# Kernel tuning notes

Measured on AMD Instinct MI355X. Metric: run time of the kernel, lower is better.

The kernel has to match this reference:

```python
import jax, jax.numpy as jnp
import numpy as np

BS, SEQ, DIN, HID, H = 2, 2048, 1024, 1024, 16
D = HID // H  # head_size = 64

def setup_inputs() -> dict:
    key = jax.random.key(0)
    ks = jax.random.split(key, 9)
    s = 0.02
    return {
        "x":    jax.random.normal(ks[0], (BS, SEQ, DIN), jnp.float32),
        "Wq":   jax.random.normal(ks[1], (DIN, HID), jnp.float32) * s,
        "bq":   jax.random.normal(ks[2], (HID,), jnp.float32) * s,
        "Wk":   jax.random.normal(ks[3], (DIN, HID), jnp.float32) * s,
        "bk":   jax.random.normal(ks[4], (HID,), jnp.float32) * s,
        "Wv":   jax.random.normal(ks[5], (DIN, HID), jnp.float32) * s,
        "bv":   jax.random.normal(ks[6], (HID,), jnp.float32) * s,
        "Wmix": jax.random.normal(ks[7], (HID, HID), jnp.float32) * s,
        "bmix": jax.random.normal(ks[8], (HID,), jnp.float32) * s,
    }

def reference(x, Wq, bq, Wk, bk, Wv, bv, Wmix, bmix):
    bs, seq, _ = x.shape
    scale = jnp.asarray(D ** 0.5, x.dtype)
    # projections, split heads: [b, s, H, D] (contiguous channel slices per head,
    # equivalent to the torch transpose/reshape dance)
    q = (x @ Wq + bq).reshape(bs, seq, H, D)
    k = (x @ Wk + bk).reshape(bs, seq, H, D)
    v = (x @ Wv + bv).reshape(bs, seq, H, D)
    scores = jnp.einsum('bqhd,bkhd->bhqk', q, k) / scale  # [b, H, seq, seq]
    causal_mask = jnp.triu(jnp.ones((seq, seq), bool), k=1)
    scores = jnp.where(causal_mask, -jnp.inf, scores)
    probs = jax.nn.softmax(scores, axis=-1)
    att = jnp.einsum('bhqk,bkhd->bqhd', probs, v).reshape(bs, seq, HID)
    return att @ Wmix + bmix
```

## Files before the change

kernel.cpp:

```cpp
#include <hip/hip_runtime.h>
#include <hip/hip_bf16.h>

#define BS 2
#define SEQ 2048
#define DIN 1024
#define HID 1024
#define NH 16
#define HD 64
#define M_ROWS (BS*SEQ)
#define NQKV 3072

typedef __attribute__((ext_vector_type(8))) short short8;
typedef __attribute__((ext_vector_type(4))) short short4v;
typedef __attribute__((ext_vector_type(8))) __bf16 bf16x8;
typedef __attribute__((ext_vector_type(4))) float floatx4;

__device__ __forceinline__ short f2bf(float f) {
  return __builtin_bit_cast(short, (__bf16)f);
}
__device__ __forceinline__ float bf2f(short s) {
  return __uint_as_float(((unsigned)(unsigned short)s) << 16);
}

__device__ __forceinline__ floatx4 mfma16(short8 a, short8 b, floatx4 c) {
  return __builtin_amdgcn_mfma_f32_16x16x32_bf16(
      __builtin_bit_cast(bf16x8, a), __builtin_bit_cast(bf16x8, b), c, 0, 0, 0);
}

__device__ __forceinline__ float exp2fast(float x) {
#if __has_builtin(__builtin_amdgcn_exp2f)
  return __builtin_amdgcn_exp2f(x);
#else
  return exp2f(x);
#endif
}

__device__ __forceinline__ void gload_lds16(const void* g, void* l) {
  __builtin_amdgcn_global_load_lds(
      (const __attribute__((address_space(1))) unsigned int*)g,
      (__attribute__((address_space(3))) unsigned int*)l, 16, 0, 0);
}

__device__ __forceinline__ void lds_w8s(short* base, int row, int colsh, short8 v) {
  *(short8*)((char*)base + row * 128 + ((colsh * 2) ^ ((row & 7) << 4))) = v;
}
__device__ __forceinline__ void lds_w4s(short* base, int row, int colsh, short4v v) {
  *(short4v*)((char*)base + row * 128 + ((colsh * 2) ^ ((row & 7) << 4))) = v;
}
__device__ __forceinline__ short8 lds_r8s(const short* base, int row, int colsh) {
  return *(const short8*)((const char*)base + row * 128 + ((colsh * 2) ^ ((row & 7) << 4)));
}

__global__ __launch_bounds__(256) void convx_kernel(const float* __restrict__ x,
                                                    short* __restrict__ xb) {
  int gid = blockIdx.x * 256 + threadIdx.x;
  const float4* x4 = (const float4*)x;
  float4 v0 = x4[2 * gid], v1 = x4[2 * gid + 1];
  short8 o;
  o[0] = f2bf(v0.x); o[1] = f2bf(v0.y); o[2] = f2bf(v0.z); o[3] = f2bf(v0.w);
  o[4] = f2bf(v1.x); o[5] = f2bf(v1.y); o[6] = f2bf(v1.z); o[7] = f2bf(v1.w);
  *(short8*)&xb[(size_t)gid * 8] = o;
}

__global__ __launch_bounds__(256) void transw_kernel(
    const float* __restrict__ Wq, const float* __restrict__ Wk,
    const float* __restrict__ Wv, const float* __restrict__ Wmix,
    short* __restrict__ Wt, short* __restrict__ Wmixt)
{
  __shared__ float Ws[64][65];
  const float* src; short* dst;
  switch (blockIdx.z) {
    case 0:  src = Wq;   dst = Wt;                 break;
    case 1:  src = Wk;   dst = Wt + (1u << 20);    break;
    case 2:  src = Wv;   dst = Wt + (2u << 20);    break;
    default: src = Wmix; dst = Wmixt;              break;
  }
  const int n0 = blockIdx.x * 64, k0 = blockIdx.y * 64;
  const int c = threadIdx.x & 63, r0 = threadIdx.x >> 6;
  #pragma unroll
  for (int i = 0; i < 16; ++i) {
    int rr = r0 + 4 * i;
    Ws[rr][c] = src[(size_t)(k0 + rr) * DIN + n0 + c];
  }
  __syncthreads();
  #pragma unroll
  for (int i = 0; i < 16; ++i) {
    int cc = r0 + 4 * i;
    dst[(size_t)(n0 + cc) * DIN + k0 + c] = f2bf(Ws[c][cc]);
  }
}

template<int BM, int BN, bool OUT_F32, bool QKV>
__global__ __launch_bounds__(256) void gemm_kernel(
    const short* __restrict__ A, const short* __restrict__ Bt,
    const float* __restrict__ bias, void* __restrict__ Cp,
    short* __restrict__ vt, int Ndim, int Kdim)
{
  constexpr int MT = BM / 32, NT = BN / 32;
  __shared__ short As[BM * 64];
  __shared__ short Bs[BN * 64];
  const int tid = threadIdx.x;
  const int wid = tid >> 6, lane = tid & 63, lg = lane >> 4, lm = lane & 15;
  const int wr = wid >> 1, wc = wid & 1;
  const int m0 = blockIdx.y * BM, n0 = blockIdx.x * BN;

  floatx4 acc[MT][NT];
  #pragma unroll
  for (int i = 0; i < MT; ++i)
    #pragma unroll
    for (int j = 0; j < NT; ++j) acc[i][j] = floatx4{0.f, 0.f, 0.f, 0.f};

  for (int k0 = 0; k0 < Kdim; k0 += 64) {
    __syncthreads();
    #pragma unroll
    for (int j = 0; j < BM / 32; ++j) {
      int flat = tid + 256 * j;
      int row = flat >> 3, ch = (flat & 7) ^ (row & 7);
      gload_lds16(A + (size_t)(m0 + row) * Kdim + k0 + ch * 8,
                  (char*)As + wid * 1024 + j * 4096);
    }
    #pragma unroll
    for (int j = 0; j < BN / 32; ++j) {
      int flat = tid + 256 * j;
      int row = flat >> 3, ch = (flat & 7) ^ (row & 7);
      gload_lds16(Bt + (size_t)(n0 + row) * Kdim + k0 + ch * 8,
                  (char*)Bs + wid * 1024 + j * 4096);
    }
    __syncthreads();

    #pragma unroll
    for (int kk = 0; kk < 2; ++kk) {
      short8 a[MT], b[NT];
      #pragma unroll
      for (int mt = 0; mt < MT; ++mt) {
        int row = wr * (BM / 2) + mt * 16 + lm;
        int ch = (kk * 4 + lg) ^ (row & 7);
        a[mt] = *(const short8*)&As[row * 64 + ch * 8];
      }
      #pragma unroll
      for (int nt = 0; nt < NT; ++nt) {
        int row = wc * (BN / 2) + nt * 16 + lm;
        int ch = (kk * 4 + lg) ^ (row & 7);
        b[nt] = *(const short8*)&Bs[row * 64 + ch * 8];
      }
      #pragma unroll
      for (int mt = 0; mt < MT; ++mt)
        #pragma unroll
        for (int nt = 0; nt < NT; ++nt)
          acc[mt][nt] = mfma16(a[mt], b[nt], acc[mt][nt]);
    }
  }

  #pragma unroll
  for (int mt = 0; mt < MT; ++mt) {
    const int row0 = m0 + wr * (BM / 2) + mt * 16 + 4 * lg;
    #pragma unroll
    for (int nt = 0; nt < NT; ++nt) {
      const int col = n0 + wc * (BN / 2) + nt * 16 + lm;
      const float bv = bias[col];
      if (QKV && n0 >= 2048) {
        int hd = col - 2048;
        int bb = row0 >> 11, s = row0 & 2047;
        short4v pv;
        #pragma unroll
        for (int r = 0; r < 4; ++r) pv[r] = f2bf(acc[mt][nt][r] + bv);
        *(short4v*)&vt[((size_t)(bb * (NH * HD) + hd)) * SEQ + s] = pv;
      } else {
        #pragma unroll
        for (int r = 0; r < 4; ++r) {
          float v = acc[mt][nt][r] + bv;
          if (OUT_F32) ((float*)Cp)[(size_t)(row0 + r) * Ndim + col] = v;
          else         ((short*)Cp)[(size_t)(row0 + r) * Ndim + col] = f2bf(v);
        }
      }
    }
  }
}

#define MFIX 12.0f
__global__ __launch_bounds__(256) void attn_kernel(
    const short* __restrict__ qkv, const short* __restrict__ vt,
    short* __restrict__ att, short* __restrict__ pO, float* __restrict__ pml)
{
  __shared__ short Ks[64 * 64];
  __shared__ short Vs[64 * 64];
  __shared__ short Ps[4 * 16 * 64];
  const int tid = threadIdx.x;
  const int wid = tid >> 6, lane = tid & 63, lg = lane >> 4, lm = lane & 15;

  int id = blockIdx.x, x, c;
  if (id < 4)        { x = id;                       c = 0;        }
  else if (id < 12)  { int t = id - 4;   x = 4  + (t >> 1); c = t & 1; }
  else if (id < 24)  { int t = id - 12;  x = 8  + t / 3;    c = t % 3; }
  else if (id < 40)  { int t = id - 24;  x = 12 + (t >> 2); c = t & 3; }
  else if (id < 60)  { int t = id - 40;  x = 16 + t / 5;    c = t % 5; }
  else if (id < 84)  { int t = id - 60;  x = 20 + t / 6;    c = t % 6; }
  else if (id < 112) { int t = id - 84;  x = 24 + t / 7;    c = t % 7; }
  else               { int t = id - 112; x = 28 + (t >> 3); c = t & 7; }
  const int nch = (x >> 2) + 1;
  const int tb = c * 4;
  const int te = min(tb + 4, x + 1);
  const int q0 = x * 64;
  const int bh = blockIdx.y, b = bh >> 4, h = bh & 15;
  const short* qp = qkv + (size_t)(b * SEQ) * NQKV + h * HD;
  const short* kp = qp + HID;
  const short* vp = vt + (size_t)bh * HD * SEQ;

  const float cl2 = 0.18033688011112042f;
  const int qrow_g = q0 + wid * 16 + lm;
  short8 qf[2];
  {
    const short* qrow = qp + (size_t)qrow_g * NQKV;
    #pragma unroll
    for (int kk = 0; kk < 2; ++kk) {
      short8 raw = *(const short8*)(qrow + kk * 32 + lg * 8);
      #pragma unroll
      for (int j = 0; j < 8; ++j) qf[kk][j] = f2bf(bf2f(raw[j]) * cl2);
    }
  }

  short8 ones;
  #pragma unroll
  for (int j = 0; j < 8; ++j) ones[j] = (short)0x3F80;

  const int rstage = tid >> 3, c8 = (tid & 7) * 8;
  short8 kreg[2], vreg[2];
  #pragma unroll
  for (int i = 0; i < 2; ++i) {
    kreg[i] = *(const short8*)(kp + (size_t)(tb * 64 + rstage + 32 * i) * NQKV + c8);
    vreg[i] = *(const short8*)(vp + (size_t)(rstage + 32 * i) * SEQ + tb * 64 + c8);
  }

  short* psw = Ps + wid * 16 * 64;
  floatx4 o[4];
  floatx4 ol = floatx4{0.f, 0.f, 0.f, 0.f};
  #pragma unroll
  for (int nt = 0; nt < 4; ++nt) o[nt] = floatx4{0.f, 0.f, 0.f, 0.f};

  for (int t = tb; t < te; ++t) {
    __syncthreads();
    #pragma unroll
    for (int i = 0; i < 2; ++i) {
      lds_w8s(Ks, rstage + 32 * i, c8, kreg[i]);
      lds_w8s(Vs, rstage + 32 * i, c8, vreg[i]);
    }
    __syncthreads();
    if (t + 1 < te) {
      const int kv1 = (t + 1) * 64;
      #pragma unroll
      for (int i = 0; i < 2; ++i) {
        kreg[i] = *(const short8*)(kp + (size_t)(kv1 + rstage + 32 * i) * NQKV + c8);
        vreg[i] = *(const short8*)(vp + (size_t)(rstage + 32 * i) * SEQ + kv1 + c8);
      }
    }

    floatx4 s[4];
    #pragma unroll
    for (int nt = 0; nt < 4; ++nt) s[nt] = floatx4{-MFIX, -MFIX, -MFIX, -MFIX};
    __builtin_amdgcn_s_setprio(1);
    #pragma unroll
    for (int kk = 0; kk < 2; ++kk)
      #pragma unroll
      for (int nt = 0; nt < 4; ++nt)
        s[nt] = mfma16(lds_r8s(Ks, nt * 16 + lm, kk * 32 + lg * 8), qf[kk], s[nt]);
    __builtin_amdgcn_s_setprio(0);

    if (t == x) {
      #pragma unroll
      for (int nt = 0; nt < 4; ++nt)
        #pragma unroll
        for (int r = 0; r < 4; ++r) {
          int kv = t * 64 + nt * 16 + 4 * lg + r;
          if (kv > qrow_g) s[nt][r] = -3e38f;
        }
    }

    #pragma unroll
    for (int nt = 0; nt < 4; ++nt) {
      short4v pv;
      #pragma unroll
      for (int r = 0; r < 4; ++r) pv[r] = f2bf(exp2fast(s[nt][r]));
      lds_w4s(psw, lm, nt * 16 + 4 * lg, pv);
    }

    #pragma unroll
    for (int kk = 0; kk < 2; ++kk) {
      short8 pf = lds_r8s(psw, lm, kk * 32 + lg * 8);
      __builtin_amdgcn_s_setprio(1);
      #pragma unroll
      for (int nt = 0; nt < 4; ++nt)
        o[nt] = mfma16(lds_r8s(Vs, nt * 16 + lm, kk * 32 + lg * 8), pf, o[nt]);
      ol = mfma16(ones, pf, ol);
      __builtin_amdgcn_s_setprio(0);
    }
  }

  if (nch == 1) {
    const float linv = 1.0f / ol[0];
    #pragma unroll
    for (int nt = 0; nt < 4; ++nt) {
      short4v ov;
      #pragma unroll
      for (int r = 0; r < 4; ++r) ov[r] = f2bf(o[nt][r] * linv);
      *(short4v*)&att[((size_t)(b * SEQ + qrow_g)) * HID + h * HD + nt * 16 + 4 * lg] = ov;
    }
  } else {
    const int g = x >> 2;
    const int slot = bh * 140 + (2 * g * g + 2 * g - 4 + (x & 3) * (g + 1)) + c;
    short* po = pO + (size_t)slot * 4096;
    const int ql = wid * 16 + lm;
    #pragma unroll
    for (int nt = 0; nt < 4; ++nt) {
      short4v ov;
      #pragma unroll
      for (int r = 0; r < 4; ++r) ov[r] = f2bf(o[nt][r]);
      *(short4v*)&po[ql * 64 + nt * 16 + 4 * lg] = ov;
    }
    if (lane < 16) {
      pml[slot * 128 + 64 + ql] = ol[0];
    }
  }
}

__global__ __launch_bounds__(256) void combine_kernel(
    const short* __restrict__ pO, const float* __restrict__ pml,
    short* __restrict__ att)
{
  const int x = 4 + blockIdx.x;
  const int bh = blockIdx.y, b = bh >> 4, h = bh & 15;
  const int g = x >> 2;
  const int nch = g + 1;
  const int tid = threadIdx.x;
  const int row = tid >> 2, d0 = (tid & 3) * 16;
  const int base_slot = bh * 140 + (2 * g * g + 2 * g - 4 + (x & 3) * (g + 1));

  float L = 0.f;
  for (int cc = 0; cc < nch; ++cc)
    L += pml[(base_slot + cc) * 128 + 64 + row];
  const float inv = 1.0f / L;

  float acc[16];
  #pragma unroll
  for (int j = 0; j < 16; ++j) acc[j] = 0.f;
  for (int cc = 0; cc < nch; ++cc) {
    const short* po = pO + (size_t)(base_slot + cc) * 4096 + row * 64 + d0;
    short8 v0 = *(const short8*)po, v1 = *(const short8*)(po + 8);
    #pragma unroll
    for (int j = 0; j < 8; ++j) {
      acc[j]     += bf2f(v0[j]);
      acc[j + 8] += bf2f(v1[j]);
    }
  }
  short8 o0, o1;
  #pragma unroll
  for (int j = 0; j < 8; ++j) {
    o0[j] = f2bf(acc[j] * inv);
    o1[j] = f2bf(acc[j + 8] * inv);
  }
  short* dst = att + ((size_t)(b * SEQ + x * 64 + row)) * HID + h * HD + d0;
  *(short8*)dst = o0;
  *(short8*)(dst + 8) = o1;
}

extern "C" void kernel_launch(void* const* d_in, const int* in_sizes, int n_in,
                              void* d_out, int out_size, void* d_ws, size_t ws_size,
                              hipStream_t stream) {
  (void)in_sizes; (void)n_in; (void)out_size; (void)ws_size;
  const float* x    = (const float*)d_in[0];
  const float* Wq   = (const float*)d_in[1];
  const float* bq   = (const float*)d_in[2];
  const float* Wk   = (const float*)d_in[3];
  const float* bk   = (const float*)d_in[4];
  const float* Wv   = (const float*)d_in[5];
  const float* bv   = (const float*)d_in[6];
  const float* Wmix = (const float*)d_in[7];
  const float* bmix = (const float*)d_in[8];
  float* out = (float*)d_out;

  char* w = (char*)d_ws;
  short* xb      = (short*)w; w += (size_t)8 << 20;
  short* Wt      = (short*)w; w += (size_t)6 << 20;
  short* Wmixt   = (short*)w; w += (size_t)2 << 20;
  float* biascat = (float*)w; w += (size_t)64 << 10;
  short* qkvb    = (short*)w; w += (size_t)24 << 20;
  short* vtb     = (short*)w; w += (size_t)8 << 20;
  short* ab      = (short*)w; w += (size_t)8 << 20;
  short* pO      = (short*)w; w += (size_t)140 * 32 * 4096 * 2;
  float* pml     = (float*)w;

  hipLaunchKernelGGL(convx_kernel, dim3(2048), dim3(256), 0, stream, x, xb);
  hipLaunchKernelGGL(transw_kernel, dim3(16, 16, 4), dim3(256), 0, stream,
                     Wq, Wk, Wv, Wmix, Wt, Wmixt);
  hipMemcpyAsync(biascat,        bq, 1024 * sizeof(float), hipMemcpyDeviceToDevice, stream);
  hipMemcpyAsync(biascat + 1024, bk, 1024 * sizeof(float), hipMemcpyDeviceToDevice, stream);
  hipMemcpyAsync(biascat + 2048, bv, 1024 * sizeof(float), hipMemcpyDeviceToDevice, stream);

  hipLaunchKernelGGL((gemm_kernel<128, 128, false, true>), dim3(NQKV / 128, M_ROWS / 128),
                     dim3(256), 0, stream, xb, Wt, biascat, (void*)qkvb, vtb, NQKV, DIN);

  hipLaunchKernelGGL(attn_kernel, dim3(144, BS * NH), dim3(256), 0, stream,
                     qkvb, vtb, ab, pO, pml);
  hipLaunchKernelGGL(combine_kernel, dim3(28, BS * NH), dim3(256), 0, stream,
                     pO, pml, ab);

  hipLaunchKernelGGL((gemm_kernel<64, 128, true, false>), dim3(HID / 128, M_ROWS / 64),
                     dim3(256), 0, stream, ab, Wmixt, bmix, (void*)out, (short*)nullptr,
                     HID, DIN);
}
```

Baseline: 115.3 us.

## Process two 64-row query tiles per attention block to reuse K/V tiles

Each attention block now handles 128 query rows, split into two 64-row sub-tiles that share every staged K/V tile in LDS. This halves the global K/V loads and LDS staging per query row, and halves the number of partial-output slots and combine blocks. The block index is now decoded by a loop instead of the hard-coded table. In exchange, each block holds twice the accumulators (more register pressure), and there are half as many blocks, so occupancy and load balance across CUs may suffer.

```diff
diff --git a/kernel.cpp b/kernel.cpp
--- a/kernel.cpp
+++ b/kernel.cpp
@@ -188,34 +188,30 @@
   const int tid = threadIdx.x;
   const int wid = tid >> 6, lane = tid & 63, lg = lane >> 4, lm = lane & 15;
 
-  int id = blockIdx.x, x, c;
-  if (id < 4)        { x = id;                       c = 0;        }
-  else if (id < 12)  { int t = id - 4;   x = 4  + (t >> 1); c = t & 1; }
-  else if (id < 24)  { int t = id - 12;  x = 8  + t / 3;    c = t % 3; }
-  else if (id < 40)  { int t = id - 24;  x = 12 + (t >> 2); c = t & 3; }
-  else if (id < 60)  { int t = id - 40;  x = 16 + t / 5;    c = t % 5; }
-  else if (id < 84)  { int t = id - 60;  x = 20 + t / 6;    c = t % 6; }
-  else if (id < 112) { int t = id - 84;  x = 24 + t / 7;    c = t % 7; }
-  else               { int t = id - 112; x = 28 + (t >> 3); c = t & 7; }
-  const int nch = (x >> 2) + 1;
+  int id = blockIdx.x, x = 0;
+  for (;;) { int n = (x >> 1) + 1; if (id < n) break; id -= n; ++x; }
+  const int c = id;
+  const int nch = (x >> 1) + 1;
+  const int ntile = 2 * x + 2;
   const int tb = c * 4;
-  const int te = min(tb + 4, x + 1);
-  const int q0 = x * 64;
+  const int te = min(tb + 4, ntile);
+  const int q0 = x * 128;
   const int bh = blockIdx.y, b = bh >> 4, h = bh & 15;
   const short* qp = qkv + (size_t)(b * SEQ) * NQKV + h * HD;
   const short* kp = qp + HID;
   const short* vp = vt + (size_t)bh * HD * SEQ;
 
   const float cl2 = 0.18033688011112042f;
-  const int qrow_g = q0 + wid * 16 + lm;
-  short8 qf[2];
-  {
-    const short* qrow = qp + (size_t)qrow_g * NQKV;
+  const int qrl = wid * 16 + lm;
+  short8 qf[2][2];
+  #pragma unroll
+  for (int sp = 0; sp < 2; ++sp) {
+    const short* qrow = qp + (size_t)(q0 + sp * 64 + qrl) * NQKV;
     #pragma unroll
     for (int kk = 0; kk < 2; ++kk) {
       short8 raw = *(const short8*)(qrow + kk * 32 + lg * 8);
       #pragma unroll
-      for (int j = 0; j < 8; ++j) qf[kk][j] = f2bf(bf2f(raw[j]) * cl2);
+      for (int j = 0; j < 8; ++j) qf[sp][kk][j] = f2bf(bf2f(raw[j]) * cl2);
     }
   }
 
@@ -232,10 +228,14 @@
   }
 
   short* psw = Ps + wid * 16 * 64;
-  floatx4 o[4];
-  floatx4 ol = floatx4{0.f, 0.f, 0.f, 0.f};
-  #pragma unroll
-  for (int nt = 0; nt < 4; ++nt) o[nt] = floatx4{0.f, 0.f, 0.f, 0.f};
+  floatx4 o[2][4];
+  floatx4 ol[2];
+  #pragma unroll
+  for (int sp = 0; sp < 2; ++sp) {
+    ol[sp] = floatx4{0.f, 0.f, 0.f, 0.f};
+    #pragma unroll
+    for (int nt = 0; nt < 4; ++nt) o[sp][nt] = floatx4{0.f, 0.f, 0.f, 0.f};
+  }
 
   for (int t = tb; t < te; ++t) {
     __syncthreads();
@@ -254,70 +254,82 @@
       }
     }
 
-    floatx4 s[4];
-    #pragma unroll
-    for (int nt = 0; nt < 4; ++nt) s[nt] = floatx4{-MFIX, -MFIX, -MFIX, -MFIX};
-    __builtin_amdgcn_s_setprio(1);
-    #pragma unroll
-    for (int kk = 0; kk < 2; ++kk)
-      #pragma unroll
-      for (int nt = 0; nt < 4; ++nt)
-        s[nt] = mfma16(lds_r8s(Ks, nt * 16 + lm, kk * 32 + lg * 8), qf[kk], s[nt]);
-    __builtin_amdgcn_s_setprio(0);
-
-    if (t == x) {
-      #pragma unroll
-      for (int nt = 0; nt < 4; ++nt)
-        #pragma unroll
-        for (int r = 0; r < 4; ++r) {
-          int kv = t * 64 + nt * 16 + 4 * lg + r;
-          if (kv > qrow_g) s[nt][r] = -3e38f;
-        }
-    }
-
-    #pragma unroll
-    for (int nt = 0; nt < 4; ++nt) {
-      short4v pv;
-      #pragma unroll
-      for (int r = 0; r < 4; ++r) pv[r] = f2bf(exp2fast(s[nt][r]));
-      lds_w4s(psw, lm, nt * 16 + 4 * lg, pv);
-    }
-
-    #pragma unroll
-    for (int kk = 0; kk < 2; ++kk) {
-      short8 pf = lds_r8s(psw, lm, kk * 32 + lg * 8);
+    #pragma unroll
+    for (int sp = 0; sp < 2; ++sp) {
+      if (sp == 0 && t == 2 * x + 1) continue;
+
+      floatx4 s[4];
+      #pragma unroll
+      for (int nt = 0; nt < 4; ++nt) s[nt] = floatx4{-MFIX, -MFIX, -MFIX, -MFIX};
       __builtin_amdgcn_s_setprio(1);
       #pragma unroll
-      for (int nt = 0; nt < 4; ++nt)
-        o[nt] = mfma16(lds_r8s(Vs, nt * 16 + lm, kk * 32 + lg * 8), pf, o[nt]);
-      ol = mfma16(ones, pf, ol);
+      for (int kk = 0; kk < 2; ++kk)
+        #pragma unroll
+        for (int nt = 0; nt < 4; ++nt)
+          s[nt] = mfma16(lds_r8s(Ks, nt * 16 + lm, kk * 32 + lg * 8), qf[sp][kk], s[nt]);
       __builtin_amdgcn_s_setprio(0);
+
+      if (t == 2 * x + sp) {
+        const int qrow_g = q0 + sp * 64 + qrl;
+        #pragma unroll
+        for (int nt = 0; nt < 4; ++nt)
+          #pragma unroll
+          for (int r = 0; r < 4; ++r) {
+            int kv = t * 64 + nt * 16 + 4 * lg + r;
+            if (kv > qrow_g) s[nt][r] = -3e38f;
+          }
+      }
+
+      #pragma unroll
+      for (int nt = 0; nt < 4; ++nt) {
+        short4v pv;
+        #pragma unroll
+        for (int r = 0; r < 4; ++r) pv[r] = f2bf(exp2fast(s[nt][r]));
+        lds_w4s(psw, lm, nt * 16 + 4 * lg, pv);
+      }
+
+      #pragma unroll
+      for (int kk = 0; kk < 2; ++kk) {
+        short8 pf = lds_r8s(psw, lm, kk * 32 + lg * 8);
+        __builtin_amdgcn_s_setprio(1);
+        #pragma unroll
+        for (int nt = 0; nt < 4; ++nt)
+          o[sp][nt] = mfma16(lds_r8s(Vs, nt * 16 + lm, kk * 32 + lg * 8), pf, o[sp][nt]);
+        ol[sp] = mfma16(ones, pf, ol[sp]);
+        __builtin_amdgcn_s_setprio(0);
+      }
     }
   }
 
   if (nch == 1) {
-    const float linv = 1.0f / ol[0];
-    #pragma unroll
-    for (int nt = 0; nt < 4; ++nt) {
-      short4v ov;
-      #pragma unroll
-      for (int r = 0; r < 4; ++r) ov[r] = f2bf(o[nt][r] * linv);
-      *(short4v*)&att[((size_t)(b * SEQ + qrow_g)) * HID + h * HD + nt * 16 + 4 * lg] = ov;
+    #pragma unroll
+    for (int sp = 0; sp < 2; ++sp) {
+      const float linv = 1.0f / ol[sp][0];
+      const int qrow_g = q0 + sp * 64 + qrl;
+      #pragma unroll
+      for (int nt = 0; nt < 4; ++nt) {
+        short4v ov;
+        #pragma unroll
+        for (int r = 0; r < 4; ++r) ov[r] = f2bf(o[sp][nt][r] * linv);
+        *(short4v*)&att[((size_t)(b * SEQ + qrow_g)) * HID + h * HD + nt * 16 + 4 * lg] = ov;
+      }
     }
   } else {
-    const int g = x >> 2;
-    const int slot = bh * 140 + (2 * g * g + 2 * g - 4 + (x & 3) * (g + 1)) + c;
-    short* po = pO + (size_t)slot * 4096;
-    const int ql = wid * 16 + lm;
-    #pragma unroll
-    for (int nt = 0; nt < 4; ++nt) {
-      short4v ov;
-      #pragma unroll
-      for (int r = 0; r < 4; ++r) ov[r] = f2bf(o[nt][r]);
-      *(short4v*)&po[ql * 64 + nt * 16 + 4 * lg] = ov;
-    }
-    if (lane < 16) {
-      pml[slot * 128 + 64 + ql] = ol[0];
+    int off = 0;
+    for (int y = 2; y < x; ++y) off += (y >> 1) + 1;
+    const int slot = bh * 70 + off + c;
+    short* po = pO + (size_t)slot * 8192;
+    #pragma unroll
+    for (int sp = 0; sp < 2; ++sp) {
+      const int ql = sp * 64 + qrl;
+      #pragma unroll
+      for (int nt = 0; nt < 4; ++nt) {
+        short4v ov;
+        #pragma unroll
+        for (int r = 0; r < 4; ++r) ov[r] = f2bf(o[sp][nt][r]);
+        *(short4v*)&po[ql * 64 + nt * 16 + 4 * lg] = ov;
+      }
+      if (lane < 16) pml[slot * 128 + ql] = ol[sp][0];
     }
   }
 }
@@ -326,40 +338,40 @@
     const short* __restrict__ pO, const float* __restrict__ pml,
     short* __restrict__ att)
 {
-  const int x = 4 + blockIdx.x;
+  const int x = 2 + blockIdx.x;
   const int bh = blockIdx.y, b = bh >> 4, h = bh & 15;
-  const int g = x >> 2;
-  const int nch = g + 1;
+  const int nch = (x >> 1) + 1;
   const int tid = threadIdx.x;
-  const int row = tid >> 2, d0 = (tid & 3) * 16;
-  const int base_slot = bh * 140 + (2 * g * g + 2 * g - 4 + (x & 3) * (g + 1));
+  const int row = tid >> 1, d0 = (tid & 1) * 32;
+  int off = 0;
+  for (int y = 2; y < x; ++y) off += (y >> 1) + 1;
+  const int base_slot = bh * 70 + off;
 
   float L = 0.f;
   for (int cc = 0; cc < nch; ++cc)
-    L += pml[(base_slot + cc) * 128 + 64 + row];
+    L += pml[(base_slot + cc) * 128 + row];
   const float inv = 1.0f / L;
 
-  float acc[16];
-  #pragma unroll
-  for (int j = 0; j < 16; ++j) acc[j] = 0.f;
+  float acc[32];
+  #pragma unroll
+  for (int j = 0; j < 32; ++j) acc[j] = 0.f;
   for (int cc = 0; cc < nch; ++cc) {
-    const short* po = pO + (size_t)(base_slot + cc) * 4096 + row * 64 + d0;
-    short8 v0 = *(const short8*)po, v1 = *(const short8*)(po + 8);
-    #pragma unroll
-    for (int j = 0; j < 8; ++j) {
-      acc[j]     += bf2f(v0[j]);
-      acc[j + 8] += bf2f(v1[j]);
-    }
-  }
-  short8 o0, o1;
-  #pragma unroll
-  for (int j = 0; j < 8; ++j) {
-    o0[j] = f2bf(acc[j] * inv);
-    o1[j] = f2bf(acc[j + 8] * inv);
-  }
-  short* dst = att + ((size_t)(b * SEQ + x * 64 + row)) * HID + h * HD + d0;
-  *(short8*)dst = o0;
-  *(short8*)(dst + 8) = o1;
+    const short* po = pO + (size_t)(base_slot + cc) * 8192 + row * 64 + d0;
+    #pragma unroll
+    for (int v = 0; v < 4; ++v) {
+      short8 vv = *(const short8*)(po + v * 8);
+      #pragma unroll
+      for (int j = 0; j < 8; ++j) acc[v * 8 + j] += bf2f(vv[j]);
+    }
+  }
+  short* dst = att + ((size_t)(b * SEQ + x * 128 + row)) * HID + h * HD + d0;
+  #pragma unroll
+  for (int v = 0; v < 4; ++v) {
+    short8 ov;
+    #pragma unroll
+    for (int j = 0; j < 8; ++j) ov[j] = f2bf(acc[v * 8 + j] * inv);
+    *(short8*)(dst + v * 8) = ov;
+  }
 }
 
 extern "C" void kernel_launch(void* const* d_in, const int* in_sizes, int n_in,
@@ -385,7 +397,7 @@
   short* qkvb    = (short*)w; w += (size_t)24 << 20;
   short* vtb     = (short*)w; w += (size_t)8 << 20;
   short* ab      = (short*)w; w += (size_t)8 << 20;
-  short* pO      = (short*)w; w += (size_t)140 * 32 * 4096 * 2;
+  short* pO      = (short*)w; w += (size_t)70 * 32 * 8192 * 2;
   float* pml     = (float*)w;
 
   hipLaunchKernelGGL(convx_kernel, dim3(2048), dim3(256), 0, stream, x, xb);
@@ -398,9 +410,9 @@
   hipLaunchKernelGGL((gemm_kernel<128, 128, false, true>), dim3(NQKV / 128, M_ROWS / 128),
                      dim3(256), 0, stream, xb, Wt, biascat, (void*)qkvb, vtb, NQKV, DIN);
 
-  hipLaunchKernelGGL(attn_kernel, dim3(144, BS * NH), dim3(256), 0, stream,
+  hipLaunchKernelGGL(attn_kernel, dim3(72, BS * NH), dim3(256), 0, stream,
                      qkvb, vtb, ab, pO, pml);
-  hipLaunchKernelGGL(combine_kernel, dim3(28, BS * NH), dim3(256), 0, stream,
+  hipLaunchKernelGGL(combine_kernel, dim3(14, BS * NH), dim3(256), 0, stream,
                      pO, pml, ab);
 
   hipLaunchKernelGGL((gemm_kernel<64, 128, true, false>), dim3(HID / 128, M_ROWS / 64),
```

Result: slower. 129.0 us (+11.9%).
